# Optimization experiments

Measured on AMD Instinct MI355X. Metric: run time of the kernel, lower is better.

## Reference

```python
import jax, jax.numpy as jnp
import numpy as np

B, D, N, F = 2048, 512, 100000, 64
NEG = -1000000.0


def setup_inputs() -> dict:
    key = jax.random.key(0)
    k1, k2, k3, k4 = jax.random.split(key, 4)
    q = jax.random.normal(k1, (B, D), dtype=jnp.float32)
    rhs = jax.random.normal(k2, (D, N), dtype=jnp.float32)
    queries = jax.random.randint(k3, (B, 3), 0, N, dtype=jnp.int64)
    filter_idx = jax.random.randint(k4, (B, F), 0, N, dtype=jnp.int64)
    return {"q": q, "rhs": rhs, "queries": queries, "filter_idx": filter_idx}


def reference(q, rhs, queries, filter_idx):
    # targets[i] = score of the true triple = q[i] . rhs[:, true_rhs[i]]
    true_rhs = queries[:, 2]                         # [B]
    targets = jnp.einsum('bd,bd->b', q, rhs[:, true_rhs].T)  # [B]

    scores = q @ rhs                                  # [B, N]

    # filtered ranking: mask out known true tails + the query's own tail
    rows = jnp.arange(scores.shape[0])[:, None]       # [B, 1]
    scores = scores.at[rows, filter_idx].set(NEG)
    scores = scores.at[jnp.arange(scores.shape[0]), true_rhs].set(NEG)

    # rank = 1 + number of candidates scoring >= the true triple
    ranks = 1.0 + jnp.sum((scores >= targets[:, None]).astype(jnp.float32), axis=1)
    return ranks
```

## Files before the change

### kernel.cpp

```cpp
#include <hip/hip_runtime.h>
#include <hip/hip_bf16.h>

#define B_ 2048
#define D_ 512
#define N_ 100000
#define F_ 64
#define NEGV (-1000000.0f)

typedef __bf16 bfx8 __attribute__((ext_vector_type(8)));
typedef float f32x4 __attribute__((ext_vector_type(4)));
typedef unsigned short u16x8 __attribute__((ext_vector_type(8)));

static __device__ __forceinline__ unsigned short f2bf(float f) {
  unsigned u = __float_as_uint(f);
  unsigned r = (u + 0x7fffu + ((u >> 16) & 1u)) >> 16;
  return (unsigned short)r;
}
static __device__ __forceinline__ float bf2f(unsigned short u) {
  return __uint_as_float(((unsigned)u) << 16);
}

static __device__ __forceinline__ void async_copy16(const void* g, void* l) {
  __builtin_amdgcn_global_load_lds((const __attribute__((address_space(1))) void*)g,
                                   (__attribute__((address_space(3))) void*)l, 16, 0, 0);
}

__global__ void targets_convert(const float* __restrict__ q, const float* __restrict__ rhs,
                                const int* __restrict__ queries, float* __restrict__ targets,
                                float* __restrict__ out, unsigned short* __restrict__ qb) {
  __shared__ float wsum[4];
  int b = blockIdx.x;
  int tid = threadIdx.x, lane = tid & 63, w = tid >> 6;
  int p = queries[b * 3 + 2];
  float2 v = ((const float2*)(q + (size_t)b * D_))[tid];
  ushort2 o; o.x = f2bf(v.x); o.y = f2bf(v.y);
  ((ushort2*)(qb + (size_t)b * D_))[tid] = o;
  float s = v.x * rhs[(size_t)(2 * tid) * N_ + p] + v.y * rhs[(size_t)(2 * tid + 1) * N_ + p];
  for (int off = 32; off; off >>= 1) s += __shfl_down(s, off, 64);
  if (lane == 0) wsum[w] = s;
  __syncthreads();
  if (tid == 0) {
    targets[b] = wsum[0] + wsum[1] + wsum[2] + wsum[3];
    out[b] = 1.0f;
  }
}

__global__ void transpose_rhs(const float* __restrict__ rhs, unsigned short* __restrict__ rt) {
  __shared__ float tile[64][65];
  int n0 = blockIdx.x * 64, d0 = blockIdx.y * 64;
  int tid = threadIdx.x;
  if (n0 + 64 <= N_) {
#pragma unroll
    for (int p = 0; p < 4; ++p) {
      int e = p * 256 + tid;
      int d = e >> 4, c4 = e & 15;
      float4 v = *(const float4*)(rhs + (size_t)(d0 + d) * N_ + n0 + c4 * 4);
      tile[d][c4 * 4 + 0] = v.x; tile[d][c4 * 4 + 1] = v.y;
      tile[d][c4 * 4 + 2] = v.z; tile[d][c4 * 4 + 3] = v.w;
    }
  } else {
    int c = tid & 63, r4 = tid >> 6;
#pragma unroll
    for (int p = 0; p < 16; ++p) {
      int d = r4 + p * 4;
      if (n0 + c < N_) tile[d][c] = rhs[(size_t)(d0 + d) * N_ + n0 + c];
    }
  }
  __syncthreads();
#pragma unroll
  for (int p = 0; p < 4; ++p) {
    int e = p * 256 + tid;
    int n = e >> 4, dg = e & 15;
    if (n0 + n < N_) {
      ushort4 o;
      o.x = f2bf(tile[dg * 4 + 0][n]);
      o.y = f2bf(tile[dg * 4 + 1][n]);
      o.z = f2bf(tile[dg * 4 + 2][n]);
      o.w = f2bf(tile[dg * 4 + 3][n]);
      *(ushort4*)(rt + (size_t)(n0 + n) * D_ + d0 + dg * 4) = o;
    }
  }
}

__global__ void __launch_bounds__(256) gemm_count(
    const unsigned short* __restrict__ qb,
    const unsigned short* __restrict__ rt,
    const float* __restrict__ targets,
    float* __restrict__ out) {
  __shared__ unsigned short As[2][128 * 32];
  __shared__ unsigned short Bs[2][128 * 32];
  __shared__ float sT[128];
  __shared__ int cnt2[2][128];

  int tid = threadIdx.x;
  int m0 = blockIdx.x * 128;
  int n0 = blockIdx.y * 128;

  if (tid < 128) sT[tid] = targets[m0 + tid];

  int w = tid >> 6, lane = tid & 63;
  int mw = (w & 1) * 64, nw = (w >> 1) * 64;
  int quad = lane >> 4, l16 = lane & 15;

  int c0 = tid, c1 = 256 + tid;
  int am0 = c0 >> 2, aj0 = (c0 & 3) * 8;
  int am1 = c1 >> 2, aj1 = (c1 & 3) * 8;
  int bn0g = n0 + am0; if (bn0g > N_ - 1) bn0g = N_ - 1;
  int bn1g = n0 + am1; if (bn1g > N_ - 1) bn1g = N_ - 1;
  const unsigned short* agp0 = qb + (size_t)(m0 + am0) * D_ + aj0;
  const unsigned short* agp1 = qb + (size_t)(m0 + am1) * D_ + aj1;
  const unsigned short* bgp0 = rt + (size_t)bn0g * D_ + aj0;
  const unsigned short* bgp1 = rt + (size_t)bn1g * D_ + aj1;

  f32x4 acc[4][4];
  f32x4 z = {0.f, 0.f, 0.f, 0.f};
#pragma unroll
  for (int i = 0; i < 4; ++i)
#pragma unroll
    for (int j = 0; j < 4; ++j) acc[i][j] = z;

  async_copy16(agp0, &As[0][c0 * 8]);
  async_copy16(agp1, &As[0][c1 * 8]);
  async_copy16(bgp0, &Bs[0][c0 * 8]);
  async_copy16(bgp1, &Bs[0][c1 * 8]);

  for (int kt = 0; kt < 16; ++kt) {
    int buf = kt & 1;
    __syncthreads();
    if (kt + 1 < 16) {
      int nb = 1 - buf, k1 = (kt + 1) * 32;
      async_copy16(agp0 + k1, &As[nb][c0 * 8]);
      async_copy16(agp1 + k1, &As[nb][c1 * 8]);
      async_copy16(bgp0 + k1, &Bs[nb][c0 * 8]);
      async_copy16(bgp1 + k1, &Bs[nb][c1 * 8]);
    }

    bfx8 a[4], b[4];
#pragma unroll
    for (int mi = 0; mi < 4; ++mi) {
      int m = mw + mi * 16 + l16;
      u16x8 au = *(const u16x8*)(&As[buf][m * 32 + quad * 8]);
      a[mi] = __builtin_bit_cast(bfx8, au);
    }
#pragma unroll
    for (int ni = 0; ni < 4; ++ni) {
      int n = nw + ni * 16 + l16;
      u16x8 bu = *(const u16x8*)(&Bs[buf][n * 32 + quad * 8]);
      b[ni] = __builtin_bit_cast(bfx8, bu);
    }
#pragma unroll
    for (int mi = 0; mi < 4; ++mi)
#pragma unroll
      for (int ni = 0; ni < 4; ++ni)
        acc[mi][ni] = __builtin_amdgcn_mfma_f32_16x16x32_bf16(a[mi], b[ni], acc[mi][ni], 0, 0, 0);
  }

#pragma unroll
  for (int mi = 0; mi < 4; ++mi) {
#pragma unroll
    for (int reg = 0; reg < 4; ++reg) {
      int rl = mw + mi * 16 + quad * 4 + reg;
      float t = sT[rl];
      int c = 0;
#pragma unroll
      for (int ni = 0; ni < 4; ++ni) {
        int col = n0 + nw + ni * 16 + l16;
        if (col < N_ && acc[mi][ni][reg] >= t) c++;
      }
      c += __shfl_xor(c, 1, 64);
      c += __shfl_xor(c, 2, 64);
      c += __shfl_xor(c, 4, 64);
      c += __shfl_xor(c, 8, 64);
      if (l16 == 0) cnt2[w >> 1][rl] = c;
    }
  }
  __syncthreads();
  if (tid < 128) {
    int tot = cnt2[0][tid] + cnt2[1][tid];
    if (tot) atomicAdd(&out[m0 + tid], (float)tot);
  }
}

__global__ void corrections(const unsigned short* __restrict__ qb,
                            const unsigned short* __restrict__ rt,
                            const int* __restrict__ queries,
                            const int* __restrict__ filt,
                            const float* __restrict__ targets,
                            float* __restrict__ out) {
  int b = blockIdx.x;
  int tid = threadIdx.x;
  int w = tid >> 6, lane = tid & 63;
  __shared__ int idx[F_ + 1];
  __shared__ unsigned char uq[F_ + 1];
  if (tid <= F_) idx[tid] = (tid < F_) ? filt[b * F_ + tid] : queries[b * 3 + 2];
  __syncthreads();
  if (tid <= F_) {
    int p = idx[tid];
    bool u = true;
    for (int j = 0; j < tid; ++j)
      if (idx[j] == p) u = false;
    uq[tid] = u;
  }
  __syncthreads();
  float t = targets[b];
  float corr = 0.f;
  u16x8 qv = ((const u16x8*)(qb + (size_t)b * D_))[lane];
  for (int ii = w; ii <= F_; ii += 8) {
    if (!uq[ii]) continue;
    int p = idx[ii];
    u16x8 rv = ((const u16x8*)(rt + (size_t)p * D_))[lane];
    float s = 0.f;
#pragma unroll
    for (int j = 0; j < 8; ++j) s += bf2f(qv[j]) * bf2f(rv[j]);
    for (int off = 32; off; off >>= 1) s += __shfl_down(s, off, 64);
    if (lane == 0)
      corr += (NEGV >= t ? 1.f : 0.f) - (s >= t ? 1.f : 0.f);
  }
  if (lane == 0 && corr != 0.f) atomicAdd(&out[b], corr);
}

__global__ void targets_init(const float* __restrict__ q, const float* __restrict__ rhs,
                             const int* __restrict__ queries, float* __restrict__ targets,
                             float* __restrict__ out) {
  __shared__ float wsum[4];
  int b = blockIdx.x;
  int tid = threadIdx.x, lane = tid & 63, w = tid >> 6;
  int p = queries[b * 3 + 2];
  float s = 0.f;
  for (int d = tid; d < D_; d += 256) s += q[b * D_ + d] * rhs[(size_t)d * N_ + p];
  for (int off = 32; off; off >>= 1) s += __shfl_down(s, off, 64);
  if (lane == 0) wsum[w] = s;
  __syncthreads();
  if (tid == 0) {
    targets[b] = wsum[0] + wsum[1] + wsum[2] + wsum[3];
    out[b] = 1.0f;
  }
}

__global__ void fallback_count(const float* __restrict__ q, const float* __restrict__ rhs,
                               const int* __restrict__ queries, const int* __restrict__ filt,
                               const float* __restrict__ targets, float* __restrict__ out) {
  int b = blockIdx.y;
  int n = blockIdx.x * 256 + threadIdx.x;
  __shared__ float qs[D_];
  __shared__ int idx[F_ + 1];
  __shared__ int cnt;
  for (int d = threadIdx.x; d < D_; d += 256) qs[d] = q[b * D_ + d];
  if (threadIdx.x < F_) idx[threadIdx.x] = filt[b * F_ + threadIdx.x];
  if (threadIdx.x == F_) idx[F_] = queries[b * 3 + 2];
  if (threadIdx.x == 0) cnt = 0;
  __syncthreads();
  if (n < N_) {
    float t = targets[b];
    float s = 0.f;
    for (int d = 0; d < D_; ++d) s += qs[d] * rhs[(size_t)d * N_ + n];
    bool member = false;
    for (int j = 0; j <= F_; ++j)
      if (idx[j] == n) member = true;
    float sv = member ? NEGV : s;
    if (sv >= t) atomicAdd(&cnt, 1);
  }
  __syncthreads();
  if (threadIdx.x == 0 && cnt) atomicAdd(&out[b], (float)cnt);
}

extern "C" void kernel_launch(void* const* d_in, const int* in_sizes, int n_in,
                              void* d_out, int out_size, void* d_ws, size_t ws_size,
                              hipStream_t stream) {
  const float* q = (const float*)d_in[0];
  const float* rhs = (const float*)d_in[1];
  const int* queries = (const int*)d_in[2];
  const int* filt = (const int*)d_in[3];
  float* out = (float*)d_out;

  char* wsb = (char*)d_ws;
  float* targets = (float*)wsb;
  unsigned short* qb = (unsigned short*)(wsb + 8192);
  unsigned short* rt = (unsigned short*)(wsb + 8192 + (size_t)B_ * D_ * 2);
  size_t need = 8192 + (size_t)B_ * D_ * 2 + (size_t)N_ * D_ * 2;

  if (ws_size >= need) {
    targets_convert<<<B_, 256, 0, stream>>>(q, rhs, queries, targets, out, qb);
    transpose_rhs<<<dim3((N_ + 63) / 64, D_ / 64), 256, 0, stream>>>(rhs, rt);
    gemm_count<<<dim3(B_ / 128, (N_ + 127) / 128), 256, 0, stream>>>(qb, rt, targets, out);
    corrections<<<B_, 512, 0, stream>>>(qb, rt, queries, filt, targets, out);
  } else {
    targets_init<<<B_, 256, 0, stream>>>(q, rhs, queries, targets, out);
    fallback_count<<<dim3((N_ + 255) / 256, B_), 256, 0, stream>>>(q, rhs, queries, filt, targets, out);
  }
}
```

Baseline: 608.0 us.

## Restructure GEMM-count kernel into 256x256 tiles with swizzled LDS and staged pipeline

Rewrites the bf16 GEMM+count kernel to use 256x256 output tiles with 512 threads and a K-step of 64. LDS is XOR-swizzled to avoid bank conflicts, and global-to-LDS async copies are interleaved with MFMA quarters separated by barriers using s_setprio. Blocks are remapped so that consecutive blocks spread across M tiles, which is meant to improve L2 reuse. The aim is to raise arithmetic intensity and MFMA utilisation, at the cost of higher register and LDS pressure and a more fragile hand-scheduled waitcnt/barrier pipeline.

```diff
diff --git a/kernel.cpp b/kernel.cpp
--- a/kernel.cpp
+++ b/kernel.cpp
@@ -6,6 +6,10 @@
 #define N_ 100000
 #define F_ 64
 #define NEGV (-1000000.0f)
+
+#define NKT 8
+#define MBLK 8
+#define NBLK 391
 
 typedef __bf16 bfx8 __attribute__((ext_vector_type(8)));
 typedef float f32x4 __attribute__((ext_vector_type(4)));
@@ -82,101 +86,158 @@
   }
 }
 
-__global__ void __launch_bounds__(256) gemm_count(
+#define STAGE_A(u, qi) async_copy16(aSrc + (size_t)(qi) * 64 * D_ + (u) * 64, \
+                                    &AsU[((u) & 1) * 16384 + (qi) * 4096 + tid * 8])
+#define STAGE_B(u, qi) async_copy16(bSrcQ[qi] + (u) * 64, \
+                                    &BsU[((u) & 1) * 16384 + (qi) * 4096 + tid * 8])
+
+#define LD_A(RQU)                                                              \
+  _Pragma("unroll") for (int mi = 0; mi < 4; ++mi)                             \
+  _Pragma("unroll") for (int ks = 0; ks < 2; ++ks) {                           \
+    int m = (RQU) * 64 + mi * 16 + l16;                                        \
+    int idx = ((m * 64 + ks * 32 + quad * 8) ^ ((m & 7) << 3));                \
+    af[mi][ks] = __builtin_bit_cast(bfx8, *(const u16x8*)&AsBuf[idx]);         \
+  }
+
+#define LD_B(NH)                                                               \
+  _Pragma("unroll") for (int ni = 0; ni < 2; ++ni)                             \
+  _Pragma("unroll") for (int ks = 0; ks < 2; ++ks) {                           \
+    int n = wc * 64 + (NH) * 32 + ni * 16 + l16;                               \
+    int idx = ((n * 64 + ks * 32 + quad * 8) ^ ((n & 7) << 3));                \
+    bf[ni][ks] = __builtin_bit_cast(bfx8, *(const u16x8*)&BsBuf[idx]);         \
+  }
+
+#define MFMA_Q(NF, NH)                                                         \
+  __builtin_amdgcn_s_setprio(1);                                               \
+  _Pragma("unroll") for (int mi = 0; mi < 4; ++mi)                             \
+  _Pragma("unroll") for (int ni = 0; ni < 2; ++ni)                             \
+  _Pragma("unroll") for (int ks = 0; ks < 2; ++ks)                             \
+    acc[NF][mi][NH][ni] = __builtin_amdgcn_mfma_f32_16x16x32_bf16(             \
+        af[mi][ks], bf[ni][ks], acc[NF][mi][NH][ni], 0, 0, 0);                 \
+  __builtin_amdgcn_s_setprio(0);
+
+#define BAR()                          \
+  asm volatile("" ::: "memory");       \
+  __builtin_amdgcn_s_barrier();        \
+  asm volatile("" ::: "memory")
+
+__global__ void __launch_bounds__(512, 2) gemm_count(
     const unsigned short* __restrict__ qb,
     const unsigned short* __restrict__ rt,
     const float* __restrict__ targets,
     float* __restrict__ out) {
-  __shared__ unsigned short As[2][128 * 32];
-  __shared__ unsigned short Bs[2][128 * 32];
-  __shared__ float sT[128];
-  __shared__ int cnt2[2][128];
+  __shared__ __align__(128) unsigned short AsU[2 * 16384];
+  __shared__ __align__(128) unsigned short BsU[2 * 16384];
+  __shared__ float sT[256];
 
   int tid = threadIdx.x;
-  int m0 = blockIdx.x * 128;
-  int n0 = blockIdx.y * 128;
-
-  if (tid < 128) sT[tid] = targets[m0 + tid];
+  int orig = blockIdx.x;
+  int wgid = (orig & 7) * (MBLK * NBLK / 8) + (orig >> 3);
+  int m0 = (wgid & 7) * 256;
+  int n0 = (wgid >> 3) * 256;
 
   int w = tid >> 6, lane = tid & 63;
-  int mw = (w & 1) * 64, nw = (w >> 1) * 64;
+  int wr = w >> 2, wc = w & 3;
   int quad = lane >> 4, l16 = lane & 15;
 
-  int c0 = tid, c1 = 256 + tid;
-  int am0 = c0 >> 2, aj0 = (c0 & 3) * 8;
-  int am1 = c1 >> 2, aj1 = (c1 & 3) * 8;
-  int bn0g = n0 + am0; if (bn0g > N_ - 1) bn0g = N_ - 1;
-  int bn1g = n0 + am1; if (bn1g > N_ - 1) bn1g = N_ - 1;
-  const unsigned short* agp0 = qb + (size_t)(m0 + am0) * D_ + aj0;
-  const unsigned short* agp1 = qb + (size_t)(m0 + am1) * D_ + aj1;
-  const unsigned short* bgp0 = rt + (size_t)bn0g * D_ + aj0;
-  const unsigned short* bgp1 = rt + (size_t)bn1g * D_ + aj1;
-
-  f32x4 acc[4][4];
+  if (tid < 256) sT[tid] = targets[m0 + tid];
+  asm volatile("s_waitcnt vmcnt(0)" ::: "memory");
+
+  int l16u = tid ^ ((tid >> 3) & 7);
+  int srow = l16u >> 3;
+  int sk = (l16u & 7) * 8;
+  const unsigned short* aSrc = qb + (size_t)(m0 + srow) * D_ + sk;
+  const unsigned short* bSrcQ[4];
+#pragma unroll
+  for (int qi = 0; qi < 4; ++qi) {
+    int n = n0 + qi * 64 + srow;
+    if (n > N_ - 1) n = N_ - 1;
+    bSrcQ[qi] = rt + (size_t)n * D_ + sk;
+  }
+
+  f32x4 acc[2][4][2][2];
   f32x4 z = {0.f, 0.f, 0.f, 0.f};
 #pragma unroll
-  for (int i = 0; i < 4; ++i)
-#pragma unroll
-    for (int j = 0; j < 4; ++j) acc[i][j] = z;
-
-  async_copy16(agp0, &As[0][c0 * 8]);
-  async_copy16(agp1, &As[0][c1 * 8]);
-  async_copy16(bgp0, &Bs[0][c0 * 8]);
-  async_copy16(bgp1, &Bs[0][c1 * 8]);
-
-  for (int kt = 0; kt < 16; ++kt) {
-    int buf = kt & 1;
-    __syncthreads();
-    if (kt + 1 < 16) {
-      int nb = 1 - buf, k1 = (kt + 1) * 32;
-      async_copy16(agp0 + k1, &As[nb][c0 * 8]);
-      async_copy16(agp1 + k1, &As[nb][c1 * 8]);
-      async_copy16(bgp0 + k1, &Bs[nb][c0 * 8]);
-      async_copy16(bgp1 + k1, &Bs[nb][c1 * 8]);
+  for (int a0 = 0; a0 < 2; ++a0)
+#pragma unroll
+    for (int a1 = 0; a1 < 4; ++a1)
+#pragma unroll
+      for (int a2 = 0; a2 < 2; ++a2)
+#pragma unroll
+        for (int a3 = 0; a3 < 2; ++a3) acc[a0][a1][a2][a3] = z;
+
+#pragma unroll
+  for (int qi = 0; qi < 4; ++qi) STAGE_A(0, qi);
+#pragma unroll
+  for (int qi = 0; qi < 4; ++qi) STAGE_B(0, qi);
+  STAGE_A(1, 0); STAGE_A(1, 3);
+  asm volatile("s_waitcnt vmcnt(2)" ::: "memory");
+  BAR();
+
+#pragma unroll 2
+  for (int t = 0; t < NKT; ++t) {
+    const unsigned short* AsBuf = &AsU[(t & 1) * 16384];
+    const unsigned short* BsBuf = &BsU[(t & 1) * 16384];
+    int u = t + 1, u2 = t + 2;
+    int rquN = wr * 3, rquF = wr + 1;
+    bfx8 af[4][2], bf[2][2];
+
+    LD_A(rquN); LD_B(0);
+    if (u < NKT) { STAGE_A(u, 1); STAGE_A(u, 2); }
+    BAR();
+    MFMA_Q(0, 0);
+    BAR();
+
+    LD_B(1);
+    if (u < NKT) { STAGE_B(u, 0); STAGE_B(u, 1); }
+    BAR();
+    MFMA_Q(0, 1);
+    BAR();
+
+    LD_A(rquF); LD_B(0);
+    if (u < NKT) { STAGE_B(u, 2); STAGE_B(u, 3); }
+    if (u2 < NKT) { STAGE_A(u2, 0); STAGE_A(u2, 3); }
+    BAR();
+    MFMA_Q(1, 0);
+    BAR();
+
+    LD_B(1);
+    BAR();
+    MFMA_Q(1, 1);
+    if (u2 < NKT) { asm volatile("s_waitcnt vmcnt(2)" ::: "memory"); }
+    else          { asm volatile("s_waitcnt vmcnt(0)" ::: "memory"); }
+    BAR();
+  }
+
+  int* scnt = (int*)BsU;
+#pragma unroll
+  for (int nf = 0; nf < 2; ++nf) {
+    int rqu = nf ? (wr + 1) : wr * 3;
+#pragma unroll
+    for (int mi = 0; mi < 4; ++mi) {
+#pragma unroll
+      for (int reg = 0; reg < 4; ++reg) {
+        int rl = rqu * 64 + mi * 16 + quad * 4 + reg;
+        float tg = sT[rl];
+        int c = 0;
+#pragma unroll
+        for (int nh = 0; nh < 2; ++nh)
+#pragma unroll
+          for (int ni = 0; ni < 2; ++ni) {
+            int col = n0 + wc * 64 + nh * 32 + ni * 16 + l16;
+            if (col < N_ && acc[nf][mi][nh][ni][reg] >= tg) c++;
+          }
+        c += __shfl_xor(c, 1, 64);
+        c += __shfl_xor(c, 2, 64);
+        c += __shfl_xor(c, 4, 64);
+        c += __shfl_xor(c, 8, 64);
+        if (l16 == 0) scnt[wc * 256 + rl] = c;
+      }
     }
-
-    bfx8 a[4], b[4];
-#pragma unroll
-    for (int mi = 0; mi < 4; ++mi) {
-      int m = mw + mi * 16 + l16;
-      u16x8 au = *(const u16x8*)(&As[buf][m * 32 + quad * 8]);
-      a[mi] = __builtin_bit_cast(bfx8, au);
-    }
-#pragma unroll
-    for (int ni = 0; ni < 4; ++ni) {
-      int n = nw + ni * 16 + l16;
-      u16x8 bu = *(const u16x8*)(&Bs[buf][n * 32 + quad * 8]);
-      b[ni] = __builtin_bit_cast(bfx8, bu);
-    }
-#pragma unroll
-    for (int mi = 0; mi < 4; ++mi)
-#pragma unroll
-      for (int ni = 0; ni < 4; ++ni)
-        acc[mi][ni] = __builtin_amdgcn_mfma_f32_16x16x32_bf16(a[mi], b[ni], acc[mi][ni], 0, 0, 0);
-  }
-
-#pragma unroll
-  for (int mi = 0; mi < 4; ++mi) {
-#pragma unroll
-    for (int reg = 0; reg < 4; ++reg) {
-      int rl = mw + mi * 16 + quad * 4 + reg;
-      float t = sT[rl];
-      int c = 0;
-#pragma unroll
-      for (int ni = 0; ni < 4; ++ni) {
-        int col = n0 + nw + ni * 16 + l16;
-        if (col < N_ && acc[mi][ni][reg] >= t) c++;
-      }
-      c += __shfl_xor(c, 1, 64);
-      c += __shfl_xor(c, 2, 64);
-      c += __shfl_xor(c, 4, 64);
-      c += __shfl_xor(c, 8, 64);
-      if (l16 == 0) cnt2[w >> 1][rl] = c;
-    }
-  }
-  __syncthreads();
-  if (tid < 128) {
-    int tot = cnt2[0][tid] + cnt2[1][tid];
+  }
+  __syncthreads();
+  if (tid < 256) {
+    int tot = scnt[tid] + scnt[256 + tid] + scnt[512 + tid] + scnt[768 + tid];
     if (tot) atomicAdd(&out[m0 + tid], (float)tot);
   }
 }
@@ -282,7 +343,7 @@
   if (ws_size >= need) {
     targets_convert<<<B_, 256, 0, stream>>>(q, rhs, queries, targets, out, qb);
     transpose_rhs<<<dim3((N_ + 63) / 64, D_ / 64), 256, 0, stream>>>(rhs, rt);
-    gemm_count<<<dim3(B_ / 128, (N_ + 127) / 128), 256, 0, stream>>>(qb, rt, targets, out);
+    gemm_count<<<MBLK * NBLK, 512, 0, stream>>>(qb, rt, targets, out);
     corrections<<<B_, 512, 0, stream>>>(qb, rt, queries, filt, targets, out);
   } else {
     targets_init<<<B_, 256, 0, stream>>>(q, rhs, queries, targets, out);
```

Measured after the change: 647.4 us. +6.5%, slower.

## Enlarge GEMM tile to 128x256 with 3-stage LDS pipeline, swizzle and block remap

Applied to the files above, without the earlier changes.

The GEMM-count kernel moves from 128x128 tiles to 128x256 tiles, so each wave now computes 128x64 outputs with 32 accumulators. The LDS double buffer becomes a 3-stage ring managed with explicit waitcnt and barrier instructions. An XOR swizzle on the LDS column layout is meant to cut bank conflicts, and the 1D grid is remapped so that neighbouring blocks are spread across XCDs. Together these aim to raise MFMA work per LDS load and hide global latency, at the cost of more registers and LDS, which can limit occupancy.

```diff
diff --git a/kernel.cpp b/kernel.cpp
--- a/kernel.cpp
+++ b/kernel.cpp
@@ -6,6 +6,11 @@
 #define N_ 100000
 #define F_ 64
 #define NEGV (-1000000.0f)
+
+#define NKT 16
+#define MT 16
+#define NT 391
+#define GRID (MT * NT)
 
 typedef __bf16 bfx8 __attribute__((ext_vector_type(8)));
 typedef float f32x4 __attribute__((ext_vector_type(4)));
@@ -82,84 +87,100 @@
   }
 }
 
-__global__ void __launch_bounds__(256) gemm_count(
+__global__ void __launch_bounds__(256, 2) gemm_count(
     const unsigned short* __restrict__ qb,
     const unsigned short* __restrict__ rt,
     const float* __restrict__ targets,
     float* __restrict__ out) {
-  __shared__ unsigned short As[2][128 * 32];
-  __shared__ unsigned short Bs[2][128 * 32];
+  __shared__ __align__(128) unsigned short As[3 * 4096];
+  __shared__ __align__(128) unsigned short Bs[3 * 8192];
   __shared__ float sT[128];
-  __shared__ int cnt2[2][128];
+  __shared__ int cnt2[4][128];
 
   int tid = threadIdx.x;
-  int m0 = blockIdx.x * 128;
-  int n0 = blockIdx.y * 128;
+  int orig = blockIdx.x;
+  int lin = (orig & 7) * (GRID / 8) + (orig >> 3);
+  int m0 = (lin & (MT - 1)) * 128;
+  int n0 = (lin / MT) * 256;
 
   if (tid < 128) sT[tid] = targets[m0 + tid];
 
   int w = tid >> 6, lane = tid & 63;
-  int mw = (w & 1) * 64, nw = (w >> 1) * 64;
   int quad = lane >> 4, l16 = lane & 15;
-
-  int c0 = tid, c1 = 256 + tid;
-  int am0 = c0 >> 2, aj0 = (c0 & 3) * 8;
-  int am1 = c1 >> 2, aj1 = (c1 & 3) * 8;
-  int bn0g = n0 + am0; if (bn0g > N_ - 1) bn0g = N_ - 1;
-  int bn1g = n0 + am1; if (bn1g > N_ - 1) bn1g = N_ - 1;
-  const unsigned short* agp0 = qb + (size_t)(m0 + am0) * D_ + aj0;
-  const unsigned short* agp1 = qb + (size_t)(m0 + am1) * D_ + aj1;
-  const unsigned short* bgp0 = rt + (size_t)bn0g * D_ + aj0;
-  const unsigned short* bgp1 = rt + (size_t)bn1g * D_ + aj1;
-
-  f32x4 acc[4][4];
+  int nw = w * 64;
+  int xq = quad ^ ((l16 >> 1) & 3);
+
+  int srow = tid >> 2;
+  int scol = ((tid & 3) ^ ((tid >> 3) & 3)) * 8;
+  const unsigned short* aC0 = qb + (size_t)(m0 + srow) * D_ + scol;
+  const unsigned short* aC1 = qb + (size_t)(m0 + 64 + srow) * D_ + scol;
+  int gn0 = n0 + srow;        if (gn0 > N_ - 1) gn0 = N_ - 1;
+  int gn1 = n0 + 64 + srow;   if (gn1 > N_ - 1) gn1 = N_ - 1;
+  int gn2 = n0 + 128 + srow;  if (gn2 > N_ - 1) gn2 = N_ - 1;
+  int gn3 = n0 + 192 + srow;  if (gn3 > N_ - 1) gn3 = N_ - 1;
+  const unsigned short* bC0 = rt + (size_t)gn0 * D_ + scol;
+  const unsigned short* bC1 = rt + (size_t)gn1 * D_ + scol;
+  const unsigned short* bC2 = rt + (size_t)gn2 * D_ + scol;
+  const unsigned short* bC3 = rt + (size_t)gn3 * D_ + scol;
+
+#define STAGE(K, SB)                                                       \
+  do {                                                                     \
+    int ko = (K) * 32;                                                     \
+    async_copy16(aC0 + ko, &As[(SB) * 4096 + tid * 8]);                    \
+    async_copy16(aC1 + ko, &As[(SB) * 4096 + (256 + tid) * 8]);            \
+    async_copy16(bC0 + ko, &Bs[(SB) * 8192 + tid * 8]);                    \
+    async_copy16(bC1 + ko, &Bs[(SB) * 8192 + (256 + tid) * 8]);            \
+    async_copy16(bC2 + ko, &Bs[(SB) * 8192 + (512 + tid) * 8]);            \
+    async_copy16(bC3 + ko, &Bs[(SB) * 8192 + (768 + tid) * 8]);            \
+  } while (0)
+
+  f32x4 acc[8][4];
   f32x4 z = {0.f, 0.f, 0.f, 0.f};
 #pragma unroll
-  for (int i = 0; i < 4; ++i)
-#pragma unroll
-    for (int j = 0; j < 4; ++j) acc[i][j] = z;
-
-  async_copy16(agp0, &As[0][c0 * 8]);
-  async_copy16(agp1, &As[0][c1 * 8]);
-  async_copy16(bgp0, &Bs[0][c0 * 8]);
-  async_copy16(bgp1, &Bs[0][c1 * 8]);
-
-  for (int kt = 0; kt < 16; ++kt) {
-    int buf = kt & 1;
-    __syncthreads();
-    if (kt + 1 < 16) {
-      int nb = 1 - buf, k1 = (kt + 1) * 32;
-      async_copy16(agp0 + k1, &As[nb][c0 * 8]);
-      async_copy16(agp1 + k1, &As[nb][c1 * 8]);
-      async_copy16(bgp0 + k1, &Bs[nb][c0 * 8]);
-      async_copy16(bgp1 + k1, &Bs[nb][c1 * 8]);
-    }
-
-    bfx8 a[4], b[4];
-#pragma unroll
-    for (int mi = 0; mi < 4; ++mi) {
-      int m = mw + mi * 16 + l16;
-      u16x8 au = *(const u16x8*)(&As[buf][m * 32 + quad * 8]);
-      a[mi] = __builtin_bit_cast(bfx8, au);
+  for (int mi = 0; mi < 8; ++mi)
+#pragma unroll
+    for (int ni = 0; ni < 4; ++ni) acc[mi][ni] = z;
+
+  STAGE(0, 0);
+  STAGE(1, 1);
+
+  int cur = 0, s2 = 2;
+  for (int kt = 0; kt < NKT; ++kt) {
+    asm volatile("s_waitcnt lgkmcnt(0)" ::: "memory");
+    __builtin_amdgcn_s_barrier();
+    if (kt == NKT - 1) { asm volatile("s_waitcnt vmcnt(0)" ::: "memory"); }
+    else               { asm volatile("s_waitcnt vmcnt(6)" ::: "memory"); }
+    if (kt + 2 < NKT) STAGE(kt + 2, s2);
+
+    const unsigned short* Ab = &As[cur * 4096];
+    const unsigned short* Bb = &Bs[cur * 8192];
+    bfx8 af[8], bf[4];
+#pragma unroll
+    for (int mi = 0; mi < 8; ++mi) {
+      int m = mi * 16 + l16;
+      af[mi] = __builtin_bit_cast(bfx8, *(const u16x8*)&Ab[m * 32 + xq * 8]);
     }
 #pragma unroll
     for (int ni = 0; ni < 4; ++ni) {
       int n = nw + ni * 16 + l16;
-      u16x8 bu = *(const u16x8*)(&Bs[buf][n * 32 + quad * 8]);
-      b[ni] = __builtin_bit_cast(bfx8, bu);
-    }
-#pragma unroll
-    for (int mi = 0; mi < 4; ++mi)
+      bf[ni] = __builtin_bit_cast(bfx8, *(const u16x8*)&Bb[n * 32 + xq * 8]);
+    }
+#pragma unroll
+    for (int mi = 0; mi < 8; ++mi)
 #pragma unroll
       for (int ni = 0; ni < 4; ++ni)
-        acc[mi][ni] = __builtin_amdgcn_mfma_f32_16x16x32_bf16(a[mi], b[ni], acc[mi][ni], 0, 0, 0);
-  }
-
-#pragma unroll
-  for (int mi = 0; mi < 4; ++mi) {
+        acc[mi][ni] = __builtin_amdgcn_mfma_f32_16x16x32_bf16(af[mi], bf[ni], acc[mi][ni], 0, 0, 0);
+
+    cur = (cur == 2) ? 0 : cur + 1;
+    s2 = (s2 == 2) ? 0 : s2 + 1;
+  }
+#undef STAGE
+
+#pragma unroll
+  for (int mi = 0; mi < 8; ++mi) {
 #pragma unroll
     for (int reg = 0; reg < 4; ++reg) {
-      int rl = mw + mi * 16 + quad * 4 + reg;
+      int rl = mi * 16 + quad * 4 + reg;
       float t = sT[rl];
       int c = 0;
 #pragma unroll
@@ -171,12 +192,12 @@
       c += __shfl_xor(c, 2, 64);
       c += __shfl_xor(c, 4, 64);
       c += __shfl_xor(c, 8, 64);
-      if (l16 == 0) cnt2[w >> 1][rl] = c;
+      if (l16 == 0) cnt2[w][rl] = c;
     }
   }
   __syncthreads();
   if (tid < 128) {
-    int tot = cnt2[0][tid] + cnt2[1][tid];
+    int tot = cnt2[0][tid] + cnt2[1][tid] + cnt2[2][tid] + cnt2[3][tid];
     if (tot) atomicAdd(&out[m0 + tid], (float)tot);
   }
 }
@@ -282,7 +303,7 @@
   if (ws_size >= need) {
     targets_convert<<<B_, 256, 0, stream>>>(q, rhs, queries, targets, out, qb);
     transpose_rhs<<<dim3((N_ + 63) / 64, D_ / 64), 256, 0, stream>>>(rhs, rt);
-    gemm_count<<<dim3(B_ / 128, (N_ + 127) / 128), 256, 0, stream>>>(qb, rt, targets, out);
+    gemm_count<<<GRID, 256, 0, stream>>>(qb, rt, targets, out);
     corrections<<<B_, 512, 0, stream>>>(qb, rt, queries, filt, targets, out);
   } else {
     targets_init<<<B_, 256, 0, stream>>>(q, rhs, queries, targets, out);
```

New measurement: 655.4 us. 1.08x slower.

## Merge prep and correction kernels into fewer launches, swizzle LDS, remap GEMM blocks

Applied to the files above, without the earlier changes.

Folds target/convert and transpose into one launch, and the correction pass into the GEMM launch, with block ranges selecting the role. This cuts the number of kernel launches and tail gaps. It also applies an XOR swizzle to the LDS tile layout to reduce bank conflicts, and remaps GEMM block order so consecutive blocks spread across M tiles, which changes cache locality. The correction blocks now run with 256 threads instead of 512, so each block does more serial work.

```diff
diff --git a/kernel.cpp b/kernel.cpp
--- a/kernel.cpp
+++ b/kernel.cpp
@@ -7,6 +7,9 @@
 #define F_ 64
 #define NEGV (-1000000.0f)
 
+#define GEMM_BLKS 12512
+#define TR_BLKS 12504
+
 typedef __bf16 bfx8 __attribute__((ext_vector_type(8)));
 typedef float f32x4 __attribute__((ext_vector_type(4)));
 typedef unsigned short u16x8 __attribute__((ext_vector_type(8)));
@@ -25,30 +28,34 @@
                                    (__attribute__((address_space(3))) void*)l, 16, 0, 0);
 }
 
-__global__ void targets_convert(const float* __restrict__ q, const float* __restrict__ rhs,
-                                const int* __restrict__ queries, float* __restrict__ targets,
-                                float* __restrict__ out, unsigned short* __restrict__ qb) {
+__global__ void prep(const float* __restrict__ q, const float* __restrict__ rhs,
+                     const int* __restrict__ queries, float* __restrict__ targets,
+                     float* __restrict__ out, unsigned short* __restrict__ qb,
+                     unsigned short* __restrict__ rt) {
+  __shared__ float tile[64][65];
   __shared__ float wsum[4];
-  int b = blockIdx.x;
-  int tid = threadIdx.x, lane = tid & 63, w = tid >> 6;
-  int p = queries[b * 3 + 2];
-  float2 v = ((const float2*)(q + (size_t)b * D_))[tid];
-  ushort2 o; o.x = f2bf(v.x); o.y = f2bf(v.y);
-  ((ushort2*)(qb + (size_t)b * D_))[tid] = o;
-  float s = v.x * rhs[(size_t)(2 * tid) * N_ + p] + v.y * rhs[(size_t)(2 * tid + 1) * N_ + p];
-  for (int off = 32; off; off >>= 1) s += __shfl_down(s, off, 64);
-  if (lane == 0) wsum[w] = s;
-  __syncthreads();
-  if (tid == 0) {
-    targets[b] = wsum[0] + wsum[1] + wsum[2] + wsum[3];
-    out[b] = 1.0f;
-  }
-}
-
-__global__ void transpose_rhs(const float* __restrict__ rhs, unsigned short* __restrict__ rt) {
-  __shared__ float tile[64][65];
-  int n0 = blockIdx.x * 64, d0 = blockIdx.y * 64;
   int tid = threadIdx.x;
+
+  if (blockIdx.x < B_) {
+    int b = blockIdx.x;
+    int lane = tid & 63, w = tid >> 6;
+    int p = queries[b * 3 + 2];
+    float2 v = ((const float2*)(q + (size_t)b * D_))[tid];
+    ushort2 o; o.x = f2bf(v.x); o.y = f2bf(v.y);
+    ((ushort2*)(qb + (size_t)b * D_))[tid] = o;
+    float s = v.x * rhs[(size_t)(2 * tid) * N_ + p] + v.y * rhs[(size_t)(2 * tid + 1) * N_ + p];
+    for (int off = 32; off; off >>= 1) s += __shfl_down(s, off, 64);
+    if (lane == 0) wsum[w] = s;
+    __syncthreads();
+    if (tid == 0) {
+      targets[b] = wsum[0] + wsum[1] + wsum[2] + wsum[3];
+      out[b] = 1.0f;
+    }
+    return;
+  }
+
+  int t = blockIdx.x - B_;
+  int n0 = (t >> 3) * 64, d0 = (t & 7) * 64;
   if (n0 + 64 <= N_) {
 #pragma unroll
     for (int p = 0; p < 4; ++p) {
@@ -82,29 +89,68 @@
   }
 }
 
-__global__ void __launch_bounds__(256) gemm_count(
+__global__ void __launch_bounds__(256) gemm_corr(
     const unsigned short* __restrict__ qb,
     const unsigned short* __restrict__ rt,
+    const int* __restrict__ queries,
+    const int* __restrict__ filt,
     const float* __restrict__ targets,
     float* __restrict__ out) {
   __shared__ unsigned short As[2][128 * 32];
   __shared__ unsigned short Bs[2][128 * 32];
   __shared__ float sT[128];
   __shared__ int cnt2[2][128];
+  __shared__ int idx[F_ + 1];
+  __shared__ unsigned char uq[F_ + 1];
 
   int tid = threadIdx.x;
-  int m0 = blockIdx.x * 128;
-  int n0 = blockIdx.y * 128;
+  int w = tid >> 6, lane = tid & 63;
+
+  if (blockIdx.x < B_) {
+    int b = blockIdx.x;
+    if (tid <= F_) idx[tid] = (tid < F_) ? filt[b * F_ + tid] : queries[b * 3 + 2];
+    __syncthreads();
+    if (tid <= F_) {
+      int p = idx[tid];
+      bool u = true;
+      for (int j = 0; j < tid; ++j)
+        if (idx[j] == p) u = false;
+      uq[tid] = u;
+    }
+    __syncthreads();
+    float t = targets[b];
+    float corr = 0.f;
+    u16x8 qv = ((const u16x8*)(qb + (size_t)b * D_))[lane];
+    for (int ii = w; ii <= F_; ii += 4) {
+      if (!uq[ii]) continue;
+      int p = idx[ii];
+      u16x8 rv = ((const u16x8*)(rt + (size_t)p * D_))[lane];
+      float s = 0.f;
+#pragma unroll
+      for (int j = 0; j < 8; ++j) s += bf2f(qv[j]) * bf2f(rv[j]);
+      for (int off = 32; off; off >>= 1) s += __shfl_down(s, off, 64);
+      if (lane == 0)
+        corr += (NEGV >= t ? 1.f : 0.f) - (s >= t ? 1.f : 0.f);
+    }
+    if (lane == 0 && corr != 0.f) atomicAdd(&out[b], corr);
+    return;
+  }
+
+  int g = blockIdx.x - B_;
+  int lin = (g & 7) * (GEMM_BLKS / 8) + (g >> 3);
+  int m0 = (lin & 15) * 128;
+  int n0 = (lin >> 4) * 128;
 
   if (tid < 128) sT[tid] = targets[m0 + tid];
 
-  int w = tid >> 6, lane = tid & 63;
   int mw = (w & 1) * 64, nw = (w >> 1) * 64;
   int quad = lane >> 4, l16 = lane & 15;
+  int xg = (quad ^ ((l16 >> 1) & 3)) * 8;
 
   int c0 = tid, c1 = 256 + tid;
-  int am0 = c0 >> 2, aj0 = (c0 & 3) * 8;
-  int am1 = c1 >> 2, aj1 = (c1 & 3) * 8;
+  int am0 = c0 >> 2, am1 = c1 >> 2;
+  int aj0 = ((c0 & 3) ^ ((c0 >> 3) & 3)) * 8;
+  int aj1 = ((c1 & 3) ^ ((c1 >> 3) & 3)) * 8;
   int bn0g = n0 + am0; if (bn0g > N_ - 1) bn0g = N_ - 1;
   int bn1g = n0 + am1; if (bn1g > N_ - 1) bn1g = N_ - 1;
   const unsigned short* agp0 = qb + (size_t)(m0 + am0) * D_ + aj0;
@@ -139,13 +185,13 @@
 #pragma unroll
     for (int mi = 0; mi < 4; ++mi) {
       int m = mw + mi * 16 + l16;
-      u16x8 au = *(const u16x8*)(&As[buf][m * 32 + quad * 8]);
+      u16x8 au = *(const u16x8*)(&As[buf][m * 32 + xg]);
       a[mi] = __builtin_bit_cast(bfx8, au);
     }
 #pragma unroll
     for (int ni = 0; ni < 4; ++ni) {
       int n = nw + ni * 16 + l16;
-      u16x8 bu = *(const u16x8*)(&Bs[buf][n * 32 + quad * 8]);
+      u16x8 bu = *(const u16x8*)(&Bs[buf][n * 32 + xg]);
       b[ni] = __builtin_bit_cast(bfx8, bu);
     }
 #pragma unroll
@@ -179,44 +225,6 @@
     int tot = cnt2[0][tid] + cnt2[1][tid];
     if (tot) atomicAdd(&out[m0 + tid], (float)tot);
   }
-}
-
-__global__ void corrections(const unsigned short* __restrict__ qb,
-                            const unsigned short* __restrict__ rt,
-                            const int* __restrict__ queries,
-                            const int* __restrict__ filt,
-                            const float* __restrict__ targets,
-                            float* __restrict__ out) {
-  int b = blockIdx.x;
-  int tid = threadIdx.x;
-  int w = tid >> 6, lane = tid & 63;
-  __shared__ int idx[F_ + 1];
-  __shared__ unsigned char uq[F_ + 1];
-  if (tid <= F_) idx[tid] = (tid < F_) ? filt[b * F_ + tid] : queries[b * 3 + 2];
-  __syncthreads();
-  if (tid <= F_) {
-    int p = idx[tid];
-    bool u = true;
-    for (int j = 0; j < tid; ++j)
-      if (idx[j] == p) u = false;
-    uq[tid] = u;
-  }
-  __syncthreads();
-  float t = targets[b];
-  float corr = 0.f;
-  u16x8 qv = ((const u16x8*)(qb + (size_t)b * D_))[lane];
-  for (int ii = w; ii <= F_; ii += 8) {
-    if (!uq[ii]) continue;
-    int p = idx[ii];
-    u16x8 rv = ((const u16x8*)(rt + (size_t)p * D_))[lane];
-    float s = 0.f;
-#pragma unroll
-    for (int j = 0; j < 8; ++j) s += bf2f(qv[j]) * bf2f(rv[j]);
-    for (int off = 32; off; off >>= 1) s += __shfl_down(s, off, 64);
-    if (lane == 0)
-      corr += (NEGV >= t ? 1.f : 0.f) - (s >= t ? 1.f : 0.f);
-  }
-  if (lane == 0 && corr != 0.f) atomicAdd(&out[b], corr);
 }
 
 __global__ void targets_init(const float* __restrict__ q, const float* __restrict__ rhs,
@@ -280,10 +288,8 @@
   size_t need = 8192 + (size_t)B_ * D_ * 2 + (size_t)N_ * D_ * 2;
 
   if (ws_size >= need) {
-    targets_convert<<<B_, 256, 0, stream>>>(q, rhs, queries, targets, out, qb);
-    transpose_rhs<<<dim3((N_ + 63) / 64, D_ / 64), 256, 0, stream>>>(rhs, rt);
-    gemm_count<<<dim3(B_ / 128, (N_ + 127) / 128), 256, 0, stream>>>(qb, rt, targets, out);
-    corrections<<<B_, 512, 0, stream>>>(qb, rt, queries, filt, targets, out);
+    prep<<<B_ + TR_BLKS, 256, 0, stream>>>(q, rhs, queries, targets, out, qb, rt);
+    gemm_corr<<<B_ + GEMM_BLKS, 256, 0, stream>>>(qb, rt, queries, filt, targets, out);
   } else {
     targets_init<<<B_, 256, 0, stream>>>(q, rhs, queries, targets, out);
     fallback_count<<<dim3((N_ + 255) / 256, B_), 256, 0, stream>>>(q, rhs, queries, filt, targets, out);
```

Result: no change. 599.4 us (-1.4%).
